# Optimization experiments

Hardware: AMD Instinct MI355X
Metric: run time of the kernel (lower is better)

## Reference

```python
import jax, jax.numpy as jnp
import numpy as np

N, E, F_NODE, F_EDGE, D, OUT, G = 32768, 98304, 32, 16, 64, 16, 64
EPS = 1e-5


def setup_inputs() -> dict:
    key = jax.random.key(0)
    ks = jax.random.split(key, 26)
    s = 0.05
    rn = lambda k, shp: jax.random.normal(k, shp, dtype=jnp.float32) * s
    return {
        "x": jax.random.normal(ks[0], (N, F_NODE), dtype=jnp.float32),
        "edge_attr": jax.random.normal(ks[1], (E, F_EDGE), dtype=jnp.float32),
        "edge_index": jax.random.randint(ks[2], (2, E), 0, N, dtype=jnp.int32),
        "batch": jnp.sort(jax.random.randint(ks[3], (N,), 0, G, dtype=jnp.int32)),
        # fc1
        "fc1_w": rn(ks[4], (F_NODE, D)), "fc1_b": jnp.zeros((D,), jnp.float32),
        # edge MLP 1 + NNConv1 root/bias
        "efc1_w1": rn(ks[5], (F_EDGE, D)), "efc1_b1": jnp.zeros((D,), jnp.float32),
        "efc1_w2": rn(ks[6], (D, D * D)), "efc1_b2": jnp.zeros((D * D,), jnp.float32),
        "root1": rn(ks[7], (D, D)), "bias1": jnp.zeros((D,), jnp.float32),
        "gn1_w": jnp.ones((D,), jnp.float32), "gn1_b": jnp.zeros((D,), jnp.float32),
        # edge MLP 2 + NNConv2 root/bias
        "efc2_w1": rn(ks[8], (F_EDGE, D)), "efc2_b1": jnp.zeros((D,), jnp.float32),
        "efc2_w2": rn(ks[9], (D, D * D)), "efc2_b2": jnp.zeros((D * D,), jnp.float32),
        "root2": rn(ks[10], (D, D)), "bias2": jnp.zeros((D,), jnp.float32),
        "gn2_w": jnp.ones((D,), jnp.float32), "gn2_b": jnp.zeros((D,), jnp.float32),
        # fc2
        "fc2_w": rn(ks[11], (D, OUT)), "fc2_b": jnp.zeros((OUT,), jnp.float32),
    }


def _nnconv(x, edge_index, edge_attr, w1, b1, w2, b2, root, bias):
    # edge MLP -> per-edge [D, D] weight
    h = jax.nn.relu(edge_attr @ w1 + b1)
    we = (h @ w2 + b2).reshape(-1, D, D)          # [E, D, D]
    src, dst = edge_index[0], edge_index[1]
    msg = jnp.einsum('ei,eio->eo', x[src], we)    # per-edge 1xD @ DxD
    agg = jax.ops.segment_sum(msg, dst, num_segments=x.shape[0])  # aggr='add'
    return agg + x @ root + bias


def _graph_layernorm(x, w, b):
    # PyG LayerNorm(mode='graph') with batch=None: global mean/std over all elems
    xc = x - x.mean()
    return xc / (jnp.std(xc) + EPS) * w + b


def _global_mean_pool(h, batch, n_graphs):
    sums = jax.ops.segment_sum(h, batch, num_segments=n_graphs)
    cnt = jax.ops.segment_sum(jnp.ones((h.shape[0],), h.dtype), batch, num_segments=n_graphs)
    return sums / jnp.clip(cnt, 1.0)[:, None]


def reference(x, edge_attr, edge_index, batch,
              fc1_w, fc1_b,
              efc1_w1, efc1_b1, efc1_w2, efc1_b2, root1, bias1, gn1_w, gn1_b,
              efc2_w1, efc2_b1, efc2_w2, efc2_b2, root2, bias2, gn2_w, gn2_b,
              fc2_w, fc2_b):
    hx = x @ fc1_w + fc1_b
    h = jax.nn.relu(_graph_layernorm(
        _nnconv(hx, edge_index, edge_attr, efc1_w1, efc1_b1, efc1_w2, efc1_b2, root1, bias1),
        gn1_w, gn1_b))
    h = jax.nn.relu(_graph_layernorm(
        _nnconv(h, edge_index, edge_attr, efc2_w1, efc2_b1, efc2_w2, efc2_b2, root2, bias2),
        gn2_w, gn2_b))
    pooled = _global_mean_pool(h, batch, G)       # [G, D]
    return pooled @ fc2_w + fc2_b                 # [G, OUT]
```

## Files before the change

### kernel.cpp

```cpp
#include <hip/hip_runtime.h>
#include <hip/hip_bf16.h>
#include <hip/hip_fp16.h>

#define NN    32768
#define EE    98304
#define FN    32
#define FEDGE 16
#define DD    64
#define OUTD  16
#define GG    64
#define EPSL  1e-5f
#define EB    192

typedef __attribute__((ext_vector_type(8))) _Float16 f16x8;
typedef __attribute__((ext_vector_type(4))) float f32x4;

__device__ __forceinline__ void gload_lds16(const void* g, void* l) {
    __builtin_amdgcn_global_load_lds(
        (const __attribute__((address_space(1))) void*)g,
        (__attribute__((address_space(3))) void*)l, 16, 0, 0);
}

__global__ __launch_bounds__(256) void k_fc1agg(const float* __restrict__ x,
                                                const float* __restrict__ w1,
                                                const float* __restrict__ b1,
                                                const float* __restrict__ root,
                                                const float* __restrict__ rbias,
                                                float* __restrict__ hx,
                                                float* __restrict__ agg) {
    __shared__ float rowbuf[4][64];
    int t = threadIdx.x, d = t & 63, wv = t >> 6;
    int n = blockIdx.x * 4 + wv;
    const float* xr = x + n * FN;
    float acc = b1[d];
    #pragma unroll
    for (int i = 0; i < FN; ++i) acc += xr[i] * w1[i * DD + d];
    hx[n * DD + d] = acc;
    rowbuf[wv][d] = acc;
    __syncthreads();
    float a0 = rbias[d], a1 = 0.f, a2 = 0.f, a3 = 0.f;
    #pragma unroll
    for (int i = 0; i < DD; i += 4) {
        a0 += rowbuf[wv][i]     * root[i * DD + d];
        a1 += rowbuf[wv][i + 1] * root[(i + 1) * DD + d];
        a2 += rowbuf[wv][i + 2] * root[(i + 2) * DD + d];
        a3 += rowbuf[wv][i + 3] * root[(i + 3) * DD + d];
    }
    agg[n * DD + d] = (a0 + a1) + (a2 + a3);
}

__global__ __launch_bounds__(256) void k_mlpprep(const float* __restrict__ ea,
                                                 const float* __restrict__ w1,
                                                 const float* __restrict__ b1,
                                                 __half* __restrict__ het,
                                                 const float* __restrict__ w2,
                                                 const float* __restrict__ b2,
                                                 __half* __restrict__ w2t) {
    __shared__ float eas[256][17];
    int t = threadIdx.x;
    int e0 = blockIdx.x * 256;
    const float4* src = (const float4*)(ea + e0 * FEDGE);
    #pragma unroll
    for (int j = 0; j < 4; ++j) {
        float4 v = src[t + 256 * j];
        int f = (t + 256 * j) * 4;
        int e = f >> 4, i = f & 15;
        eas[e][i] = v.x; eas[e][i + 1] = v.y; eas[e][i + 2] = v.z; eas[e][i + 3] = v.w;
    }
    if (blockIdx.x < 65) {
        int s = blockIdx.x;
        const float* psrc = (s < 64) ? (w2 + s * 4096) : b2;
        int o = t >> 2;
        #pragma unroll
        for (int j = 0; j < 16; ++j) {
            int i = (t & 3) * 16 + j;
            w2t[s * 4096 + o * 64 + (i ^ ((o & 7) << 3))] = __float2half_rn(psrc[i * 64 + o]);
        }
    }
    __syncthreads();
    int e = e0 + t;
    float a[FEDGE];
    #pragma unroll
    for (int i = 0; i < FEDGE; ++i) a[i] = eas[t][i];
    for (int k = 0; k < DD; ++k) {
        float acc = b1[k];
        #pragma unroll
        for (int i = 0; i < FEDGE; ++i) acc += a[i] * w1[i * DD + k];
        acc = fmaxf(acc, 0.0f);
        het[k * EE + e] = __float2half_rn(acc);
    }
    het[DD * EE + e] = __float2half_rn(1.0f);
}

__global__ __launch_bounds__(256, 2) void k_conv(const float* __restrict__ xs,
                                                 const __half* __restrict__ het,
                                                 const __half* __restrict__ w2t,
                                                 const int* __restrict__ ei,
                                                 float* __restrict__ agg,
                                                 float* __restrict__ zbuf,
                                                 int zn) {
    __shared__ __align__(16) __half hs[65 * EB];
    __shared__ __align__(16) __half w2s[4 * 4096];

    const int t   = threadIdx.x;
    const int l   = t & 63;
    const int w   = t >> 6;
    const int wm  = w & 1;
    const int wn  = w >> 1;
    const int q   = l >> 4;
    const int r16 = l & 15;
    const int q8  = q * 8;
    const int e0  = blockIdx.x * EB;

    if (blockIdx.x == 0) {
        for (int i = t; i < zn; i += 256) zbuf[i] = 0.0f;
    }

    __half2 xh[6][8];
    #pragma unroll
    for (int sm = 0; sm < 6; ++sm) {
        int em = e0 + wm * 96 + sm * 16 + r16;
        int sn = ei[em];
        const float4* xr = (const float4*)(xs + sn * DD);
        float4 a0 = xr[q * 2], a1 = xr[q * 2 + 1];
        float4 b0 = xr[8 + q * 2], b1 = xr[8 + q * 2 + 1];
        xh[sm][0] = __floats2half2_rn(a0.x, a0.y);
        xh[sm][1] = __floats2half2_rn(a0.z, a0.w);
        xh[sm][2] = __floats2half2_rn(a1.x, a1.y);
        xh[sm][3] = __floats2half2_rn(a1.z, a1.w);
        xh[sm][4] = __floats2half2_rn(b0.x, b0.y);
        xh[sm][5] = __floats2half2_rn(b0.z, b0.w);
        xh[sm][6] = __floats2half2_rn(b1.x, b1.y);
        xh[sm][7] = __floats2half2_rn(b1.z, b1.w);
    }

    auto stage = [&](int s) {
        #pragma unroll
        for (int c = 0; c < 2; ++c)
            gload_lds16(w2t + s * 4096 + w * 1024 + c * 512 + l * 8,
                        &w2s[(s & 3) * 4096 + w * 1024 + c * 512]);
    };

    stage(0); stage(1); stage(2);

    for (int j = t; j < 65 * 24; j += 256) {
        int row = j / 24, col = j - row * 24;
        ((uint4*)hs)[j] = ((const uint4*)(het + row * EE + e0))[col];
    }
    asm volatile("s_waitcnt lgkmcnt(0)" ::: "memory");

    uint boff[2][2];
    #pragma unroll
    for (int j = 0; j < 2; ++j) {
        int o = (wn * 2 + j) * 16 + r16;
        int xm = (o & 7) << 3;
        #pragma unroll
        for (int p = 0; p < 2; ++p)
            boff[p][j] = (uint)(o * 64 + ((p * 32 + q8) ^ xm));
    }

    f32x4 acc[6][2];
    #pragma unroll
    for (int sm = 0; sm < 6; ++sm)
        #pragma unroll
        for (int j = 0; j < 2; ++j)
            acc[sm][j] = (f32x4){0.f, 0.f, 0.f, 0.f};

    for (int s = 0; s < 65; ++s) {
        __builtin_amdgcn_s_barrier();
        if (s < 62) {
            stage(s + 3);
            asm volatile("s_waitcnt vmcnt(6)" ::: "memory");
        } else {
            asm volatile("s_waitcnt vmcnt(0)" ::: "memory");
        }
        __builtin_amdgcn_s_barrier();
        __builtin_amdgcn_sched_barrier(0);

        const __half* bp = &w2s[(s & 3) * 4096];

        __half2 hh[6];
        #pragma unroll
        for (int sm = 0; sm < 6; ++sm)
            hh[sm] = __half2half2(hs[s * EB + wm * 96 + sm * 16 + r16]);

        #pragma unroll
        for (int p = 0; p < 2; ++p) {
            f16x8 bfr[2];
            #pragma unroll
            for (int j = 0; j < 2; ++j)
                bfr[j] = *(const f16x8*)(bp + boff[p][j]);
            #pragma unroll
            for (int sm = 0; sm < 6; ++sm) {
                union { f16x8 v; __half2 h2[4]; } af;
                #pragma unroll
                for (int jj = 0; jj < 4; ++jj)
                    af.h2[jj] = __hmul2(hh[sm], xh[sm][p * 4 + jj]);
                #pragma unroll
                for (int j = 0; j < 2; ++j)
                    acc[sm][j] = __builtin_amdgcn_mfma_f32_16x16x32_f16(
                        af.v, bfr[j], acc[sm][j], 0, 0, 0);
            }
        }
    }

    #pragma unroll
    for (int sm = 0; sm < 6; ++sm) {
        #pragma unroll
        for (int rr = 0; rr < 4; ++rr) {
            int em = e0 + wm * 96 + sm * 16 + q * 4 + rr;
            int dn = ei[EE + em];
            float* ar = agg + dn * DD + wn * 32 + r16;
            #pragma unroll
            for (int j = 0; j < 2; ++j)
                atomicAdd(ar + j * 16, acc[sm][j][rr]);
        }
    }
}

__global__ __launch_bounds__(256) void k_lnred(const float* __restrict__ v,
                                               float* __restrict__ stats) {
    int t = threadIdx.x;
    int base = blockIdx.x * 4096 + t;
    float s = 0.0f, s2 = 0.0f;
    #pragma unroll
    for (int j = 0; j < 16; ++j) {
        float x = v[base + j * 256];
        s += x; s2 += x * x;
    }
    #pragma unroll
    for (int off = 32; off > 0; off >>= 1) {
        s  += __shfl_down(s, off, 64);
        s2 += __shfl_down(s2, off, 64);
    }
    __shared__ float ps[8];
    int w = t >> 6;
    if ((t & 63) == 0) { ps[w] = s; ps[4 + w] = s2; }
    __syncthreads();
    if (t == 0) {
        atomicAdd(&stats[0], ps[0] + ps[1] + ps[2] + ps[3]);
        atomicAdd(&stats[1], ps[4] + ps[5] + ps[6] + ps[7]);
    }
}

__global__ __launch_bounds__(256) void k_lnagg(float* __restrict__ h1,
                                               const float* __restrict__ stats,
                                               const float* __restrict__ gw,
                                               const float* __restrict__ gb,
                                               const float* __restrict__ root,
                                               const float* __restrict__ rbias,
                                               float* __restrict__ agg2) {
    const float M = (float)(NN * DD);
    float mean = stats[0] / M;
    float var  = stats[1] / M - mean * mean;
    float rden = 1.0f / (sqrtf(fmaxf(var, 0.0f)) + EPSL);
    __shared__ float rowbuf[4][64];
    int t = threadIdx.x, d = t & 63, wv = t >> 6;
    int n = blockIdx.x * 4 + wv;
    float v = h1[n * DD + d];
    float h = fmaxf((v - mean) * rden * gw[d] + gb[d], 0.0f);
    h1[n * DD + d] = h;
    rowbuf[wv][d] = h;
    __syncthreads();
    float a0 = rbias[d], a1 = 0.f, a2 = 0.f, a3 = 0.f;
    #pragma unroll
    for (int i = 0; i < DD; i += 4) {
        a0 += rowbuf[wv][i]     * root[i * DD + d];
        a1 += rowbuf[wv][i + 1] * root[(i + 1) * DD + d];
        a2 += rowbuf[wv][i + 2] * root[(i + 2) * DD + d];
        a3 += rowbuf[wv][i + 3] * root[(i + 3) * DD + d];
    }
    agg2[n * DD + d] = (a0 + a1) + (a2 + a3);
}

__global__ __launch_bounds__(256) void k_lnpool(const float* __restrict__ v,
                                                const float* __restrict__ stats,
                                                const float* __restrict__ gw,
                                                const float* __restrict__ gb,
                                                const int* __restrict__ batch,
                                                float* __restrict__ pool,
                                                float* __restrict__ cnt) {
    const float M = (float)(NN * DD);
    float mean = stats[0] / M;
    float var  = stats[1] / M - mean * mean;
    float rden = 1.0f / (sqrtf(fmaxf(var, 0.0f)) + EPSL);
    int t = threadIdx.x;
    int d = t & 63;
    int ln = t >> 6;
    int n0 = blockIdx.x * 256;
    float gwd = gw[d] * rden, gbd = gb[d];
    float s = 0.0f, sc = 0.0f;
    int cur = batch[n0 + ln];
    for (int j = 0; j < 64; ++j) {
        int n = n0 + ln + j * 4;
        int b = batch[n];
        if (b != cur) {
            atomicAdd(&pool[cur * DD + d], s);
            if (d == 0) atomicAdd(&cnt[cur], sc);
            s = 0.0f; sc = 0.0f; cur = b;
        }
        s  += fmaxf((v[n * DD + d] - mean) * gwd + gbd, 0.0f);
        sc += 1.0f;
    }
    atomicAdd(&pool[cur * DD + d], s);
    if (d == 0) atomicAdd(&cnt[cur], sc);
}

__global__ __launch_bounds__(256) void k_fc2(const float* __restrict__ pool,
                                             const float* __restrict__ cnt,
                                             const float* __restrict__ w,
                                             const float* __restrict__ b,
                                             float* __restrict__ out) {
    int t = threadIdx.x;
    int o = t & 15;
    int g0 = t >> 4;
    #pragma unroll
    for (int gg = 0; gg < 4; ++gg) {
        int g = g0 + gg * 16;
        float inv = 1.0f / fmaxf(cnt[g], 1.0f);
        float acc = b[o];
        #pragma unroll
        for (int d = 0; d < DD; ++d)
            acc += pool[g * DD + d] * inv * w[d * OUTD + o];
        out[g * OUTD + o] = acc;
    }
}

extern "C" void kernel_launch(void* const* d_in, const int* in_sizes, int n_in,
                              void* d_out, int out_size, void* d_ws, size_t ws_size,
                              hipStream_t stream) {
    const float* x       = (const float*)d_in[0];
    const float* ea      = (const float*)d_in[1];
    const int*   ei      = (const int*)d_in[2];
    const int*   batch   = (const int*)d_in[3];
    const float* fc1_w   = (const float*)d_in[4];
    const float* fc1_b   = (const float*)d_in[5];
    const float* e1w1    = (const float*)d_in[6];
    const float* e1b1    = (const float*)d_in[7];
    const float* e1w2    = (const float*)d_in[8];
    const float* e1b2    = (const float*)d_in[9];
    const float* root1   = (const float*)d_in[10];
    const float* bias1   = (const float*)d_in[11];
    const float* gn1w    = (const float*)d_in[12];
    const float* gn1b    = (const float*)d_in[13];
    const float* e2w1    = (const float*)d_in[14];
    const float* e2b1    = (const float*)d_in[15];
    const float* e2w2    = (const float*)d_in[16];
    const float* e2b2    = (const float*)d_in[17];
    const float* root2   = (const float*)d_in[18];
    const float* bias2   = (const float*)d_in[19];
    const float* gn2w    = (const float*)d_in[20];
    const float* gn2b    = (const float*)d_in[21];
    const float* fc2_w   = (const float*)d_in[22];
    const float* fc2_b   = (const float*)d_in[23];
    float* out = (float*)d_out;

    char* ws = (char*)d_ws;
    float*  hx    = (float*)(ws);
    float*  agg1  = (float*)(ws + 8388608);
    __half* het   = (__half*)(ws + 16777216);
    __half* w2t   = (__half*)(ws + 29556736);
    float*  pool  = (float*)(ws + 30089216);
    float*  cnt   = (float*)(ws + 30105600);
    float*  stats = (float*)(ws + 30105856);
    float*  agg2  = hx;

    k_fc1agg<<<NN / 4, 256, 0, stream>>>(x, fc1_w, fc1_b, root1, bias1, hx, agg1);
    k_mlpprep<<<EE / 256, 256, 0, stream>>>(ea, e1w1, e1b1, het, e1w2, e1b2, w2t);
    k_conv<<<EE / EB, 256, 0, stream>>>(hx, het, w2t, ei, agg1, stats, 2);
    k_lnred<<<(NN * DD) / 4096, 256, 0, stream>>>(agg1, stats);
    k_lnagg<<<NN / 4, 256, 0, stream>>>(agg1, stats, gn1w, gn1b, root2, bias2, agg2);

    k_mlpprep<<<EE / 256, 256, 0, stream>>>(ea, e2w1, e2b1, het, e2w2, e2b2, w2t);
    k_conv<<<EE / EB, 256, 0, stream>>>(agg1, het, w2t, ei, agg2, pool, 4096 + 64 + 4);
    k_lnred<<<(NN * DD) / 4096, 256, 0, stream>>>(agg2, stats + 2);

    k_lnpool<<<NN / 256, 256, 0, stream>>>(agg2, stats + 2, gn2w, gn2b, batch, pool, cnt);
    k_fc2<<<1, 256, 0, stream>>>(pool, cnt, fc2_w, fc2_b, out);
}
```

Baseline: 386.0 us.

## Load edge-MLP weights directly from global into registers, shrink edge block

```diff
diff --git a/kernel.cpp b/kernel.cpp
--- a/kernel.cpp
+++ b/kernel.cpp
@@ -10,16 +10,10 @@
 #define OUTD  16
 #define GG    64
 #define EPSL  1e-5f
-#define EB    192
+#define EB    128
 
 typedef __attribute__((ext_vector_type(8))) _Float16 f16x8;
 typedef __attribute__((ext_vector_type(4))) float f32x4;
-
-__device__ __forceinline__ void gload_lds16(const void* g, void* l) {
-    __builtin_amdgcn_global_load_lds(
-        (const __attribute__((address_space(1))) void*)g,
-        (__attribute__((address_space(3))) void*)l, 16, 0, 0);
-}
 
 __global__ __launch_bounds__(256) void k_fc1agg(const float* __restrict__ x,
                                                 const float* __restrict__ w1,
@@ -74,7 +68,7 @@
         #pragma unroll
         for (int j = 0; j < 16; ++j) {
             int i = (t & 3) * 16 + j;
-            w2t[s * 4096 + o * 64 + (i ^ ((o & 7) << 3))] = __float2half_rn(psrc[i * 64 + o]);
+            w2t[s * 4096 + o * 64 + i] = __float2half_rn(psrc[i * 64 + o]);
         }
     }
     __syncthreads();
@@ -92,7 +86,7 @@
     het[DD * EE + e] = __float2half_rn(1.0f);
 }
 
-__global__ __launch_bounds__(256, 2) void k_conv(const float* __restrict__ xs,
+__global__ __launch_bounds__(256, 3) void k_conv(const float* __restrict__ xs,
                                                  const __half* __restrict__ het,
                                                  const __half* __restrict__ w2t,
                                                  const int* __restrict__ ei,
@@ -100,7 +94,6 @@
                                                  float* __restrict__ zbuf,
                                                  int zn) {
     __shared__ __align__(16) __half hs[65 * EB];
-    __shared__ __align__(16) __half w2s[4 * 4096];
 
     const int t   = threadIdx.x;
     const int l   = t & 63;
@@ -109,17 +102,16 @@
     const int wn  = w >> 1;
     const int q   = l >> 4;
     const int r16 = l & 15;
-    const int q8  = q * 8;
     const int e0  = blockIdx.x * EB;
 
     if (blockIdx.x == 0) {
         for (int i = t; i < zn; i += 256) zbuf[i] = 0.0f;
     }
 
-    __half2 xh[6][8];
-    #pragma unroll
-    for (int sm = 0; sm < 6; ++sm) {
-        int em = e0 + wm * 96 + sm * 16 + r16;
+    __half2 xh[4][8];
+    #pragma unroll
+    for (int sm = 0; sm < 4; ++sm) {
+        int em = e0 + wm * 64 + sm * 16 + r16;
         int sn = ei[em];
         const float4* xr = (const float4*)(xs + sn * DD);
         float4 a0 = xr[q * 2], a1 = xr[q * 2 + 1];
@@ -134,64 +126,43 @@
         xh[sm][7] = __floats2half2_rn(b1.z, b1.w);
     }
 
-    auto stage = [&](int s) {
-        #pragma unroll
-        for (int c = 0; c < 2; ++c)
-            gload_lds16(w2t + s * 4096 + w * 1024 + c * 512 + l * 8,
-                        &w2s[(s & 3) * 4096 + w * 1024 + c * 512]);
-    };
-
-    stage(0); stage(1); stage(2);
-
-    for (int j = t; j < 65 * 24; j += 256) {
-        int row = j / 24, col = j - row * 24;
+    for (int j = t; j < 65 * 16; j += 256) {
+        int row = j >> 4, col = j & 15;
         ((uint4*)hs)[j] = ((const uint4*)(het + row * EE + e0))[col];
     }
-    asm volatile("s_waitcnt lgkmcnt(0)" ::: "memory");
-
-    uint boff[2][2];
-    #pragma unroll
-    for (int j = 0; j < 2; ++j) {
-        int o = (wn * 2 + j) * 16 + r16;
-        int xm = (o & 7) << 3;
+    __syncthreads();
+
+    int boffe[2][2];
+    #pragma unroll
+    for (int j = 0; j < 2; ++j)
         #pragma unroll
         for (int p = 0; p < 2; ++p)
-            boff[p][j] = (uint)(o * 64 + ((p * 32 + q8) ^ xm));
-    }
-
-    f32x4 acc[6][2];
-    #pragma unroll
-    for (int sm = 0; sm < 6; ++sm)
+            boffe[j][p] = ((wn * 2 + j) * 16 + r16) * 64 + p * 32 + q * 8;
+
+    f32x4 acc[4][2];
+    #pragma unroll
+    for (int sm = 0; sm < 4; ++sm)
         #pragma unroll
         for (int j = 0; j < 2; ++j)
             acc[sm][j] = (f32x4){0.f, 0.f, 0.f, 0.f};
 
-    for (int s = 0; s < 65; ++s) {
-        __builtin_amdgcn_s_barrier();
-        if (s < 62) {
-            stage(s + 3);
-            asm volatile("s_waitcnt vmcnt(6)" ::: "memory");
-        } else {
-            asm volatile("s_waitcnt vmcnt(0)" ::: "memory");
-        }
-        __builtin_amdgcn_s_barrier();
-        __builtin_amdgcn_sched_barrier(0);
-
-        const __half* bp = &w2s[(s & 3) * 4096];
-
-        __half2 hh[6];
-        #pragma unroll
-        for (int sm = 0; sm < 6; ++sm)
-            hh[sm] = __half2half2(hs[s * EB + wm * 96 + sm * 16 + r16]);
-
-        #pragma unroll
-        for (int p = 0; p < 2; ++p) {
-            f16x8 bfr[2];
+    auto loadB = [&](f16x8 (&B)[2][2], const __half* wp) {
+        #pragma unroll
+        for (int j = 0; j < 2; ++j)
             #pragma unroll
-            for (int j = 0; j < 2; ++j)
-                bfr[j] = *(const f16x8*)(bp + boff[p][j]);
+            for (int p = 0; p < 2; ++p)
+                B[j][p] = *(const f16x8*)(wp + boffe[j][p]);
+    };
+
+    auto compute = [&](int s, f16x8 (&B)[2][2]) {
+        __half2 hh[4];
+        #pragma unroll
+        for (int sm = 0; sm < 4; ++sm)
+            hh[sm] = __half2half2(hs[s * EB + wm * 64 + sm * 16 + r16]);
+        #pragma unroll
+        for (int p = 0; p < 2; ++p)
             #pragma unroll
-            for (int sm = 0; sm < 6; ++sm) {
+            for (int sm = 0; sm < 4; ++sm) {
                 union { f16x8 v; __half2 h2[4]; } af;
                 #pragma unroll
                 for (int jj = 0; jj < 4; ++jj)
@@ -199,16 +170,27 @@
                 #pragma unroll
                 for (int j = 0; j < 2; ++j)
                     acc[sm][j] = __builtin_amdgcn_mfma_f32_16x16x32_f16(
-                        af.v, bfr[j], acc[sm][j], 0, 0, 0);
+                        af.v, B[j][p], acc[sm][j], 0, 0, 0);
             }
-        }
-    }
-
-    #pragma unroll
-    for (int sm = 0; sm < 6; ++sm) {
+    };
+
+    f16x8 BA[2][2], BB[2][2];
+    const __half* wp = w2t;
+    loadB(BA, wp);
+    for (int s = 0; s < 64; s += 2) {
+        loadB(BB, wp + 4096);
+        compute(s, BA);
+        loadB(BA, wp + 8192);
+        compute(s + 1, BB);
+        wp += 8192;
+    }
+    compute(64, BA);
+
+    #pragma unroll
+    for (int sm = 0; sm < 4; ++sm) {
         #pragma unroll
         for (int rr = 0; rr < 4; ++rr) {
-            int em = e0 + wm * 96 + sm * 16 + q * 4 + rr;
+            int em = e0 + wm * 64 + sm * 16 + q * 4 + rr;
             int dn = ei[EE + em];
             float* ar = agg + dn * DD + wn * 32 + r16;
             #pragma unroll
```

New measurement: 458.2 us. +18.7%, slower.
